# Kernel optimization log

Measured on AMD Instinct MI355X. Metric: run time of the kernel, lower is better.

## Reference

```python
import jax, jax.numpy as jnp
import numpy as np

N = 100000   # nodes
E = 800000   # edges (avg degree 8)
F = 64       # node feature dim
H = 64       # hidden units


def setup_inputs() -> dict:
    key = jax.random.key(0)
    ks = jax.random.split(key, 18)
    s = 0.05  # weight scale
    inp = {
        "node_feat": jax.random.normal(ks[0], (N, F), jnp.float32),
        "edge_weight": jax.random.uniform(ks[1], (E,), jnp.float32),
        "hidden_state": jax.random.normal(ks[2], (N, H), jnp.float32),
        "W_z": jax.random.normal(ks[3], (F, H), jnp.float32) * s,
        "b_z": jnp.zeros((H,), jnp.float32),
        "W_r": jax.random.normal(ks[4], (F, H), jnp.float32) * s,
        "b_r": jnp.zeros((H,), jnp.float32),
        "W_h": jax.random.normal(ks[5], (F, H), jnp.float32) * s,
        "b_h": jnp.zeros((H,), jnp.float32),
        "Wl_z": jax.random.normal(ks[6], (2 * H, H), jnp.float32) * s,
        "bl_z": jnp.zeros((H,), jnp.float32),
        "Wl_r": jax.random.normal(ks[7], (2 * H, H), jnp.float32) * s,
        "bl_r": jnp.zeros((H,), jnp.float32),
        "Wl_h": jax.random.normal(ks[8], (2 * H, H), jnp.float32) * s,
        "bl_h": jnp.zeros((H,), jnp.float32),
        "W_out": jax.random.normal(ks[9], (H, F), jnp.float32) * s,
        "b_out": jnp.zeros((F,), jnp.float32),
        "edge_index": jax.random.randint(ks[10], (2, E), 0, N, dtype=jnp.int64),
    }
    return inp


def _gcn(x, W, b, src, dst, w):
    # GCN-style graph conv with given (pre-normalized) edge weights:
    # out[v] = sum_{(u->v)} w_e * (x[u] @ W) + b
    m = x @ W                                   # [N, H] transform first (cheaper)
    msgs = m[src] * w[:, None]                  # [E, H] gather + scale
    return jax.ops.segment_sum(msgs, dst, num_segments=N) + b


def reference(node_feat, edge_weight, hidden_state,
              W_z, b_z, W_r, b_r, W_h, b_h,
              Wl_z, bl_z, Wl_r, bl_r, Wl_h, bl_h,
              W_out, b_out, edge_index):
    src, dst = edge_index[0], edge_index[1]
    # TGCN GRU gates
    cz = _gcn(node_feat, W_z, b_z, src, dst, edge_weight)          # [N, H]
    z = jax.nn.sigmoid(jnp.concatenate([cz, hidden_state], -1) @ Wl_z + bl_z)
    cr = _gcn(node_feat, W_r, b_r, src, dst, edge_weight)
    r = jax.nn.sigmoid(jnp.concatenate([cr, hidden_state], -1) @ Wl_r + bl_r)
    ch = _gcn(node_feat, W_h, b_h, src, dst, edge_weight)
    h_tilde = jnp.tanh(jnp.concatenate([ch, hidden_state * r], -1) @ Wl_h + bl_h)
    h = z * hidden_state + (1.0 - z) * h_tilde                     # [N, H]
    # readout
    y = jax.nn.relu(h) @ W_out + b_out                             # [N, F]
    return (y, h)
```

## Files before the change

kernel.cpp:

```cpp
#include <hip/hip_runtime.h>
#include <hip/hip_bf16.h>
#include <math.h>


typedef __attribute__((ext_vector_type(8))) short bf16x8;
typedef __attribute__((ext_vector_type(4))) float f32x4;

static __device__ __forceinline__ short f2bf(float x) {
    union { float f; unsigned u; } v; v.f = x;
    unsigned r = v.u + 0x7fffu + ((v.u >> 16) & 1u);
    return (short)(r >> 16);
}
static __device__ __forceinline__ float bf2f(short s) {
    return __uint_as_float((unsigned)(unsigned short)s << 16);
}
__device__ __forceinline__ float sigmoid_(float x) { return 1.0f / (1.0f + __expf(-x)); }
__device__ __forceinline__ float tanh_(float x)    { return 1.0f - 2.0f / (__expf(2.0f * x) + 1.0f); }

__global__ __launch_bounds__(256) void prep_zero_kernel(
    short* __restrict__ AXb, int n16)
{
    int i = blockIdx.x * 256 + threadIdx.x;
    const uint4 z = make_uint4(0, 0, 0, 0);
    if (i < n16) ((uint4*)AXb)[i] = z;
}

__global__ __launch_bounds__(256) void fuse_weights_kernel(
    const float* __restrict__ Wz, const float* __restrict__ Wr, const float* __restrict__ Wh,
    const float* __restrict__ bz, const float* __restrict__ br, const float* __restrict__ bh,
    const float* __restrict__ Wlz, const float* __restrict__ Wlr, const float* __restrict__ Wlh,
    const float* __restrict__ blz, const float* __restrict__ blr, const float* __restrict__ blh,
    const float* __restrict__ Wout, const float* __restrict__ bout_,
    short* __restrict__ WT, float* __restrict__ bfv)
{
    int g = blockIdx.x;
    int tid = threadIdx.x;
    if (g == 3) {
        for (int i = tid; i < 4096; i += 256) {
            int k = i >> 6, n = i & 63;
            WT[6 * 4096 + n * 64 + k] = f2bf(Wout[k * 64 + n]);
        }
        if (tid < 64) bfv[192 + tid] = bout_[tid];
        return;
    }
    const float* Win = (g == 0) ? Wz : (g == 1) ? Wr : Wh;
    const float* Wl  = (g == 0) ? Wlz : (g == 1) ? Wlr : Wlh;
    const float* b   = (g == 0) ? bz : (g == 1) ? br : bh;
    const float* bl  = (g == 0) ? blz : (g == 1) ? blr : blh;

    __shared__ float wl_s[64][65];
    for (int i = tid; i < 4096; i += 256) wl_s[i >> 6][i & 63] = Wl[i];
    __syncthreads();

    int k = tid >> 2;
    int j0 = (tid & 3) << 4;
    float acc[16];
#pragma unroll
    for (int jj = 0; jj < 16; jj++) acc[jj] = 0.f;
    for (int t = 0; t < 64; t++) {
        float a = Win[k * 64 + t];
#pragma unroll
        for (int jj = 0; jj < 16; jj++) acc[jj] = fmaf(a, wl_s[t][j0 + jj], acc[jj]);
    }
#pragma unroll
    for (int jj = 0; jj < 16; jj++) WT[g * 4096 + (j0 + jj) * 64 + k] = f2bf(acc[jj]);

    for (int i = tid; i < 4096; i += 256) {
        int kk = i >> 6, n = i & 63;
        WT[(3 + g) * 4096 + n * 64 + kk] = f2bf(Wl[(64 + kk) * 64 + n]);
    }
    if (tid < 64) {
        float a2 = bl[tid];
        for (int t = 0; t < 64; t++) a2 = fmaf(b[t], wl_s[t][tid], a2);
        bfv[g * 64 + tid] = a2;
    }
}

__global__ __launch_bounds__(256) void scatter_kernel(
    const float* __restrict__ x, const float* __restrict__ ew,
    const int* __restrict__ ei, short* __restrict__ AXb, int E)
{
    int e  = (blockIdx.x * 256 + threadIdx.x) >> 5;
    int lj = threadIdx.x & 31;
    if (e < E) {
        int src = ei[e];
        int dst = ei[E + e];
        float w = ew[e];
        float2 xv = *(const float2*)(x + (size_t)src * 64 + lj * 2);
        unsigned pk = (unsigned)(unsigned short)f2bf(xv.x * w)
                    | ((unsigned)(unsigned short)f2bf(xv.y * w) << 16);
        short* addr = AXb + (size_t)dst * 64 + lj * 2;
        asm volatile("global_atomic_pk_add_bf16 %0, %1, off"
                     :: "v"(addr), "v"(pk) : "memory");
    }
    asm volatile("s_waitcnt vmcnt(0)" ::: "memory");
}

__global__ __launch_bounds__(256) void gates_kernel(
    const short* __restrict__ AXb, const float* __restrict__ hid,
    const short* __restrict__ WT, const float* __restrict__ bfv,
    float* __restrict__ outY, float* __restrict__ outH, int nNodes)
{
    __shared__ short axs[64][72];
    __shared__ short hs [64][72];
    __shared__ short rsb[64][72];

    const int tid  = threadIdx.x;
    const int w    = tid >> 6;
    const int lane = tid & 63;
    const int lr   = lane & 15;
    const int lg   = lane >> 4;
    const int col  = w * 16 + lr;
    const int n0   = blockIdx.x * 64;

    {
        int row = tid >> 2;
        int c0  = (tid & 3) << 4;
        int n   = n0 + row;
        bool valid = n < nNodes;
        const float4 z4 = make_float4(0.f, 0.f, 0.f, 0.f);
        const bf16x8 zb = {0, 0, 0, 0, 0, 0, 0, 0};
        bf16x8 a0 = valid ? *(const bf16x8*)(AXb + (size_t)n * 64 + c0)     : zb;
        bf16x8 a1 = valid ? *(const bf16x8*)(AXb + (size_t)n * 64 + c0 + 8) : zb;
        *(bf16x8*)(&axs[row][c0])     = a0;
        *(bf16x8*)(&axs[row][c0 + 8]) = a1;
#pragma unroll
        for (int q = 0; q < 4; q++) {
            float4 vh = valid ? *(const float4*)(hid + (size_t)n * 64 + c0 + q * 4) : z4;
            int c = c0 + q * 4;
            hs[row][c + 0] = f2bf(vh.x); hs[row][c + 1] = f2bf(vh.y);
            hs[row][c + 2] = f2bf(vh.z); hs[row][c + 3] = f2bf(vh.w);
        }
    }

    bf16x8 wf[7][2];
#pragma unroll
    for (int m = 0; m < 7; m++)
#pragma unroll
        for (int kb = 0; kb < 2; kb++)
            wf[m][kb] = *(const bf16x8*)(WT + m * 4096 + col * 64 + kb * 32 + lg * 8);
    const float bz_ = bfv[col], br_ = bfv[64 + col], bh_ = bfv[128 + col], bo_ = bfv[192 + col];

    __syncthreads();

    const f32x4 zero4 = {0.f, 0.f, 0.f, 0.f};
    f32x4 accz[4], accr[4], acch[4];
#pragma unroll
    for (int rt = 0; rt < 4; rt++) { accz[rt] = zero4; accr[rt] = zero4; acch[rt] = zero4; }

#pragma unroll
    for (int rt = 0; rt < 4; rt++) {
        int arow = rt * 16 + lr;
#pragma unroll
        for (int kb = 0; kb < 2; kb++) {
            bf16x8 aa = *(const bf16x8*)(&axs[arow][kb * 32 + lg * 8]);
            bf16x8 ah = *(const bf16x8*)(&hs [arow][kb * 32 + lg * 8]);
            accz[rt] = __builtin_amdgcn_mfma_f32_16x16x32_bf16(aa, wf[0][kb], accz[rt], 0, 0, 0);
            accr[rt] = __builtin_amdgcn_mfma_f32_16x16x32_bf16(aa, wf[1][kb], accr[rt], 0, 0, 0);
            acch[rt] = __builtin_amdgcn_mfma_f32_16x16x32_bf16(aa, wf[2][kb], acch[rt], 0, 0, 0);
            accz[rt] = __builtin_amdgcn_mfma_f32_16x16x32_bf16(ah, wf[3][kb], accz[rt], 0, 0, 0);
            accr[rt] = __builtin_amdgcn_mfma_f32_16x16x32_bf16(ah, wf[4][kb], accr[rt], 0, 0, 0);
        }
    }

    float zf[16];
#pragma unroll
    for (int rt = 0; rt < 4; rt++) {
#pragma unroll
        for (int i = 0; i < 4; i++) {
            int row = rt * 16 + lg * 4 + i;
            float z = sigmoid_(accz[rt][i] + bz_);
            float r = sigmoid_(accr[rt][i] + br_);
            zf[rt * 4 + i] = z;
            rsb[row][col] = f2bf(r * bf2f(hs[row][col]));
        }
    }
    __syncthreads();

#pragma unroll
    for (int rt = 0; rt < 4; rt++) {
        int arow = rt * 16 + lr;
#pragma unroll
        for (int kb = 0; kb < 2; kb++) {
            bf16x8 ar = *(const bf16x8*)(&rsb[arow][kb * 32 + lg * 8]);
            acch[rt] = __builtin_amdgcn_mfma_f32_16x16x32_bf16(ar, wf[5][kb], acch[rt], 0, 0, 0);
        }
    }
#pragma unroll
    for (int rt = 0; rt < 4; rt++) {
#pragma unroll
        for (int i = 0; i < 4; i++) {
            int row = rt * 16 + lg * 4 + i;
            float ht = tanh_(acch[rt][i] + bh_);
            float z  = zf[rt * 4 + i];
            float hv = z * bf2f(hs[row][col]) + (1.f - z) * ht;
            int n = n0 + row;
            if (n < nNodes) outH[(size_t)n * 64 + col] = hv;
            axs[row][col] = f2bf(fmaxf(hv, 0.f));
        }
    }
    __syncthreads();

    f32x4 accy[4];
#pragma unroll
    for (int rt = 0; rt < 4; rt++) accy[rt] = zero4;
#pragma unroll
    for (int rt = 0; rt < 4; rt++) {
        int arow = rt * 16 + lr;
#pragma unroll
        for (int kb = 0; kb < 2; kb++) {
            bf16x8 aa = *(const bf16x8*)(&axs[arow][kb * 32 + lg * 8]);
            accy[rt] = __builtin_amdgcn_mfma_f32_16x16x32_bf16(aa, wf[6][kb], accy[rt], 0, 0, 0);
        }
    }
#pragma unroll
    for (int rt = 0; rt < 4; rt++) {
#pragma unroll
        for (int i = 0; i < 4; i++) {
            int row = rt * 16 + lg * 4 + i;
            int n = n0 + row;
            if (n < nNodes) outY[(size_t)n * 64 + col] = accy[rt][i] + bo_;
        }
    }
}

extern "C" void kernel_launch(void* const* d_in, const int* in_sizes, int n_in,
                              void* d_out, int out_size, void* d_ws, size_t ws_size,
                              hipStream_t stream)
{
    const float* node_feat = (const float*)d_in[0];
    const float* edge_w    = (const float*)d_in[1];
    const float* hidden    = (const float*)d_in[2];
    const float* W_z  = (const float*)d_in[3];
    const float* b_z  = (const float*)d_in[4];
    const float* W_r  = (const float*)d_in[5];
    const float* b_r  = (const float*)d_in[6];
    const float* W_h  = (const float*)d_in[7];
    const float* b_h  = (const float*)d_in[8];
    const float* Wl_z = (const float*)d_in[9];
    const float* bl_z = (const float*)d_in[10];
    const float* Wl_r = (const float*)d_in[11];
    const float* bl_r = (const float*)d_in[12];
    const float* Wl_h = (const float*)d_in[13];
    const float* bl_h = (const float*)d_in[14];
    const float* W_out = (const float*)d_in[15];
    const float* b_out = (const float*)d_in[16];
    const int*   edge_index = (const int*)d_in[17];

    const int N = in_sizes[0] / 64;
    const int E = in_sizes[1];

    char* ws = (char*)d_ws;
    size_t off = 0;
    short* AXb = (short*)(ws + off); off += (size_t)N * 64 * 2;
    short* WT  = (short*)(ws + off); off += 7 * 4096 * 2;
    float* bfv = (float*)(ws + off); off += 4 * 64 * 4;

    float* outY = (float*)d_out;
    float* outH = outY + (size_t)N * 64;

    prep_zero_kernel<<<(N * 8 + 255) / 256, 256, 0, stream>>>(AXb, N * 8);
    fuse_weights_kernel<<<4, 256, 0, stream>>>(W_z, W_r, W_h, b_z, b_r, b_h,
                                               Wl_z, Wl_r, Wl_h, bl_z, bl_r, bl_h,
                                               W_out, b_out, WT, bfv);
    scatter_kernel<<<(E * 32 + 255) / 256, 256, 0, stream>>>(
        node_feat, edge_w, edge_index, AXb, E);

    int nblk = (N + 63) / 64;
    gates_kernel<<<nblk, 256, 0, stream>>>(AXb, hidden, WT, bfv, outY, outH, N);
}
```

Before: 152.4 us.

## Replicate bf16 aggregation buffer to spread scatter atomics; fuse zeroing into weight prep

The edge scatter now accumulates into up to eight replicas of the node aggregation buffer, choosing the replica by block index, so atomics to the same destination row are spread across copies. The gates kernel sums the replicas in fp32 before converting to bf16. The separate zeroing kernel is folded into the weight-fusion kernel as extra grid-stride blocks, removing one launch. In exchange, zeroing and reading the aggregation buffer cost up to eight times more memory traffic, and the larger footprint weakens cache locality for the atomics.

```diff
diff --git a/kernel.cpp b/kernel.cpp
--- a/kernel.cpp
+++ b/kernel.cpp
@@ -17,24 +17,24 @@
 __device__ __forceinline__ float sigmoid_(float x) { return 1.0f / (1.0f + __expf(-x)); }
 __device__ __forceinline__ float tanh_(float x)    { return 1.0f - 2.0f / (__expf(2.0f * x) + 1.0f); }
 
-__global__ __launch_bounds__(256) void prep_zero_kernel(
-    short* __restrict__ AXb, int n16)
-{
-    int i = blockIdx.x * 256 + threadIdx.x;
-    const uint4 z = make_uint4(0, 0, 0, 0);
-    if (i < n16) ((uint4*)AXb)[i] = z;
-}
-
-__global__ __launch_bounds__(256) void fuse_weights_kernel(
+__global__ __launch_bounds__(256) void prep_fuse_kernel(
     const float* __restrict__ Wz, const float* __restrict__ Wr, const float* __restrict__ Wh,
     const float* __restrict__ bz, const float* __restrict__ br, const float* __restrict__ bh,
     const float* __restrict__ Wlz, const float* __restrict__ Wlr, const float* __restrict__ Wlh,
     const float* __restrict__ blz, const float* __restrict__ blr, const float* __restrict__ blh,
     const float* __restrict__ Wout, const float* __restrict__ bout_,
-    short* __restrict__ WT, float* __restrict__ bfv)
+    short* __restrict__ WT, float* __restrict__ bfv,
+    short* __restrict__ AXrep, int n16total)
 {
     int g = blockIdx.x;
     int tid = threadIdx.x;
+    if (g >= 4) {
+        int i = (g - 4) * 256 + tid;
+        int stride = (gridDim.x - 4) * 256;
+        const uint4 z = make_uint4(0, 0, 0, 0);
+        for (; i < n16total; i += stride) ((uint4*)AXrep)[i] = z;
+        return;
+    }
     if (g == 3) {
         for (int i = tid; i < 4096; i += 256) {
             int k = i >> 6, n = i & 63;
@@ -78,7 +78,8 @@
 
 __global__ __launch_bounds__(256) void scatter_kernel(
     const float* __restrict__ x, const float* __restrict__ ew,
-    const int* __restrict__ ei, short* __restrict__ AXb, int E)
+    const int* __restrict__ ei, short* __restrict__ AXrep,
+    int E, int N, int repMask)
 {
     int e  = (blockIdx.x * 256 + threadIdx.x) >> 5;
     int lj = threadIdx.x & 31;
@@ -89,7 +90,8 @@
         float2 xv = *(const float2*)(x + (size_t)src * 64 + lj * 2);
         unsigned pk = (unsigned)(unsigned short)f2bf(xv.x * w)
                     | ((unsigned)(unsigned short)f2bf(xv.y * w) << 16);
-        short* addr = AXb + (size_t)dst * 64 + lj * 2;
+        size_t rep = (size_t)(blockIdx.x & repMask);
+        short* addr = AXrep + (rep * N + dst) * 64 + lj * 2;
         asm volatile("global_atomic_pk_add_bf16 %0, %1, off"
                      :: "v"(addr), "v"(pk) : "memory");
     }
@@ -97,7 +99,8 @@
 }
 
 __global__ __launch_bounds__(256) void gates_kernel(
-    const short* __restrict__ AXb, const float* __restrict__ hid,
+    const short* __restrict__ AXrep, int nrep,
+    const float* __restrict__ hid,
     const short* __restrict__ WT, const float* __restrict__ bfv,
     float* __restrict__ outY, float* __restrict__ outH, int nNodes)
 {
@@ -119,11 +122,23 @@
         int n   = n0 + row;
         bool valid = n < nNodes;
         const float4 z4 = make_float4(0.f, 0.f, 0.f, 0.f);
-        const bf16x8 zb = {0, 0, 0, 0, 0, 0, 0, 0};
-        bf16x8 a0 = valid ? *(const bf16x8*)(AXb + (size_t)n * 64 + c0)     : zb;
-        bf16x8 a1 = valid ? *(const bf16x8*)(AXb + (size_t)n * 64 + c0 + 8) : zb;
-        *(bf16x8*)(&axs[row][c0])     = a0;
-        *(bf16x8*)(&axs[row][c0 + 8]) = a1;
+        float axf[16];
+#pragma unroll
+        for (int j = 0; j < 16; j++) axf[j] = 0.f;
+        if (valid) {
+            for (int r = 0; r < nrep; r++) {
+                const short* base = AXrep + ((size_t)r * nNodes + n) * 64 + c0;
+                bf16x8 a0 = *(const bf16x8*)(base);
+                bf16x8 a1 = *(const bf16x8*)(base + 8);
+#pragma unroll
+                for (int j = 0; j < 8; j++) {
+                    axf[j]     += bf2f(a0[j]);
+                    axf[8 + j] += bf2f(a1[j]);
+                }
+            }
+        }
+#pragma unroll
+        for (int j = 0; j < 16; j++) axs[row][c0 + j] = f2bf(axf[j]);
 #pragma unroll
         for (int q = 0; q < 4; q++) {
             float4 vh = valid ? *(const float4*)(hid + (size_t)n * 64 + c0 + q * 4) : z4;
@@ -252,20 +267,27 @@
 
     char* ws = (char*)d_ws;
     size_t off = 0;
-    short* AXb = (short*)(ws + off); off += (size_t)N * 64 * 2;
     short* WT  = (short*)(ws + off); off += 7 * 4096 * 2;
     float* bfv = (float*)(ws + off); off += 4 * 64 * 4;
+    off = (off + 127) & ~(size_t)127;
+
+    int nrep = 8;
+    while (nrep > 1 && off + (size_t)nrep * N * 128 > ws_size) nrep >>= 1;
+    short* AXrep = (short*)(ws + off);
 
     float* outY = (float*)d_out;
     float* outH = outY + (size_t)N * 64;
 
-    prep_zero_kernel<<<(N * 8 + 255) / 256, 256, 0, stream>>>(AXb, N * 8);
-    fuse_weights_kernel<<<4, 256, 0, stream>>>(W_z, W_r, W_h, b_z, b_r, b_h,
-                                               Wl_z, Wl_r, Wl_h, bl_z, bl_r, bl_h,
-                                               W_out, b_out, WT, bfv);
+    int n16total = nrep * N * 8;
+    int zblk = 4096;
+    prep_fuse_kernel<<<4 + zblk, 256, 0, stream>>>(
+        W_z, W_r, W_h, b_z, b_r, b_h, Wl_z, Wl_r, Wl_h, bl_z, bl_r, bl_h,
+        W_out, b_out, WT, bfv, AXrep, n16total);
+
     scatter_kernel<<<(E * 32 + 255) / 256, 256, 0, stream>>>(
-        node_feat, edge_w, edge_index, AXb, E);
+        node_feat, edge_w, edge_index, AXrep, E, N, nrep - 1);
 
     int nblk = (N + 63) / 64;
-    gates_kernel<<<nblk, 256, 0, stream>>>(AXb, hidden, WT, bfv, outY, outH, N);
-}
+    gates_kernel<<<nblk, 256, 0, stream>>>(AXrep, nrep, hidden,
+                                           WT, bfv, outY, outH, N);
+}
```

Result: slower. 168.0 us (+10.2%).
